# Kernel optimization log

Measured on AMD Instinct MI355X. Metric: run time of the kernel, lower is better.

The kernel has to match this reference:

```python
import jax, jax.numpy as jnp
import numpy as np

B, IN, H, E, N_EP, V_DIM = 4096, 1024, 16, 256, 2048, 64


def setup_inputs() -> dict:
    key = jax.random.key(0)
    k_x, k_c, k_w, k_k, k_v = jax.random.split(key, 5)
    x = jax.random.normal(k_x, (B, IN), dtype=jnp.float32)
    curiosity_score = jax.random.normal(k_c, (B,), dtype=jnp.float32)
    # toqueries: Linear(IN, E*H, bias=False); store as [IN, E*H] for x @ Wq
    Wq = jax.random.normal(k_w, (IN, E * H), dtype=jnp.float32) * (1.0 / np.sqrt(IN))
    # offline_keys [n_episodes, emb_size]; buffer repeats over heads (identical), so keep 2D
    keys = jax.random.normal(k_k, (N_EP, E), dtype=jnp.float32)
    # values buffer = offline_values.abs().mean(dim=-1) -> [n_episodes]
    offline_values = jax.random.normal(k_v, (N_EP, V_DIM), dtype=jnp.float32)
    values = jnp.abs(offline_values).mean(axis=-1)
    return {"x": x, "curiosity_score": curiosity_score, "Wq": Wq, "keys": keys, "values": values}


def reference(x, curiosity_score, Wq, keys, values):
    b = x.shape[0]
    # queries: [b, h, e], scaled by e**(1/4) (keys left unscaled, as in source)
    q = (x @ Wq).reshape(b, H, E) / (E ** 0.25)
    # dot: [b, h, n_episodes]; keys identical across heads -> single contraction
    dot = jnp.einsum("bhe,ne->bhn", q, keys) + values[None, None, :]
    dot = jax.nn.softmax(dot, axis=-1)
    # curiosity reweighting: scale probabilities then re-softmax (not scale-invariant)
    cur = jnp.exp(curiosity_score).reshape(b, 1, 1)
    dot = jax.nn.softmax(dot * cur, axis=-1)
    # head-mean -> [b, n_episodes]
    return dot.mean(axis=1)
```

## Files before the change

### kernel.cpp

```cpp
#include <hip/hip_runtime.h>


typedef __attribute__((ext_vector_type(8))) short bf16x8;
typedef __attribute__((ext_vector_type(4))) float f32x4;

typedef const __attribute__((address_space(1))) void* gcptr;
typedef __attribute__((address_space(3))) void* sptr;

__device__ __forceinline__ void gload16(const void* g, void* l) {
  __builtin_amdgcn_global_load_lds((gcptr)g, (sptr)l, 16, 0, 0);
}

__device__ __forceinline__ unsigned short f2bf(float f) {
  unsigned int u = __float_as_uint(f);
  unsigned int r = (u + 0x7fffu + ((u >> 16) & 1u)) >> 16;
  return (unsigned short)r;
}
__device__ __forceinline__ float bf2f(unsigned short s) {
  return __uint_as_float(((unsigned int)s) << 16);
}

__global__ void k_split(const float* __restrict__ src,
                        unsigned short* __restrict__ hi,
                        unsigned short* __restrict__ lo, int n4) {
  int i = blockIdx.x * blockDim.x + threadIdx.x;
  if (i >= n4) return;
  float4 v = reinterpret_cast<const float4*>(src)[i];
  ushort4 h, l;
  h.x = f2bf(v.x); l.x = f2bf(v.x - bf2f(h.x));
  h.y = f2bf(v.y); l.y = f2bf(v.y - bf2f(h.y));
  h.z = f2bf(v.z); l.z = f2bf(v.z - bf2f(h.z));
  h.w = f2bf(v.w); l.w = f2bf(v.w - bf2f(h.w));
  reinterpret_cast<ushort4*>(hi)[i] = h;
  reinterpret_cast<ushort4*>(lo)[i] = l;
}

__global__ void k_prepk(const float* __restrict__ keys,
                        unsigned short* __restrict__ th,
                        unsigned short* __restrict__ tl) {
  int g = blockIdx.x * blockDim.x + threadIdx.x;
  int k0 = g >> 13, rem = g & 8191;
  int jg = rem >> 6, lam = rem & 63;
  int row = jg * 16 + (lam & 15);
  int col = k0 * 32 + (lam >> 4) * 8;
  const float* s = keys + (size_t)row * 256 + col;
  float4 v0 = *reinterpret_cast<const float4*>(s);
  float4 v1 = *reinterpret_cast<const float4*>(s + 4);
  ushort4 h0, h1, l0, l1;
  h0.x = f2bf(v0.x); l0.x = f2bf(v0.x - bf2f(h0.x));
  h0.y = f2bf(v0.y); l0.y = f2bf(v0.y - bf2f(h0.y));
  h0.z = f2bf(v0.z); l0.z = f2bf(v0.z - bf2f(h0.z));
  h0.w = f2bf(v0.w); l0.w = f2bf(v0.w - bf2f(h0.w));
  h1.x = f2bf(v1.x); l1.x = f2bf(v1.x - bf2f(h1.x));
  h1.y = f2bf(v1.y); l1.y = f2bf(v1.y - bf2f(h1.y));
  h1.z = f2bf(v1.z); l1.z = f2bf(v1.z - bf2f(h1.z));
  h1.w = f2bf(v1.w); l1.w = f2bf(v1.w - bf2f(h1.w));
  reinterpret_cast<ushort4*>(th + (size_t)g * 8)[0] = h0;
  reinterpret_cast<ushort4*>(th + (size_t)g * 8)[1] = h1;
  reinterpret_cast<ushort4*>(tl + (size_t)g * 8)[0] = l0;
  reinterpret_cast<ushort4*>(tl + (size_t)g * 8)[1] = l1;
}

__global__ void k_twq(const float* __restrict__ W,
                      unsigned short* __restrict__ th,
                      unsigned short* __restrict__ tl) {
  __shared__ float t[64][65];
  int tx = threadIdx.x & 63, ty = threadIdx.x >> 6;
  int c0 = blockIdx.x * 64, r0 = blockIdx.y * 64;
#pragma unroll
  for (int i = 0; i < 64; i += 4)
    t[ty + i][tx] = W[(size_t)(r0 + ty + i) * 4096 + (c0 + tx)] * 0.25f;
  __syncthreads();
#pragma unroll
  for (int i = 0; i < 64; i += 4) {
    float v = t[tx][ty + i];
    unsigned short h = f2bf(v);
    unsigned short l = f2bf(v - bf2f(h));
    size_t o = (size_t)(c0 + ty + i) * 1024 + (r0 + tx);
    th[o] = h; tl[o] = l;
  }
}

__global__ __launch_bounds__(256) void k_gemm1(
    const unsigned short* __restrict__ Ah, const unsigned short* __restrict__ Al,
    const unsigned short* __restrict__ Bh, const unsigned short* __restrict__ Bl,
    unsigned short* __restrict__ Qh, unsigned short* __restrict__ Ql) {
  __shared__ unsigned short As[2][128][32];
  __shared__ unsigned short Bs[2][128][32];
  const int tid = threadIdx.x;
  const int w = tid >> 6, l = tid & 63;
  const int lr = l & 15, lg = l >> 4;
  const int m0 = blockIdx.y * 128, n0 = blockIdx.x * 128;
  const int wr = (w >> 1) * 64, wc = (w & 1) * 64;
  const int srow = tid >> 2;
  const int skel = (tid & 3) * 8;
  f32x4 acc[4][4] = {};

  const size_t gaBase = (size_t)(m0 + srow) * 1024 + skel;
  const size_t gbBase = (size_t)(n0 + srow) * 1024 + skel;
  char* lA0 = (char*)&As[0][0][0] + w * 1024;
  char* lA1 = (char*)&As[1][0][0] + w * 1024;
  char* lB0 = (char*)&Bs[0][0][0] + w * 1024;
  char* lB1 = (char*)&Bs[1][0][0] + w * 1024;

  for (int k0 = 0; k0 < 1024; k0 += 32) {
    gload16(Ah + gaBase + k0,             lA0);
    gload16(Ah + gaBase + 64 * 1024 + k0, lA0 + 4096);
    gload16(Al + gaBase + k0,             lA1);
    gload16(Al + gaBase + 64 * 1024 + k0, lA1 + 4096);
    gload16(Bh + gbBase + k0,             lB0);
    gload16(Bh + gbBase + 64 * 1024 + k0, lB0 + 4096);
    gload16(Bl + gbBase + k0,             lB1);
    gload16(Bl + gbBase + 64 * 1024 + k0, lB1 + 4096);
    __syncthreads();
    bf16x8 ah[4], am[4], bh[4], bm[4];
#pragma unroll
    for (int i = 0; i < 4; ++i) {
      ah[i] = *reinterpret_cast<const bf16x8*>(&As[0][wr + i * 16 + lr][lg * 8]);
      am[i] = *reinterpret_cast<const bf16x8*>(&As[1][wr + i * 16 + lr][lg * 8]);
      bh[i] = *reinterpret_cast<const bf16x8*>(&Bs[0][wc + i * 16 + lr][lg * 8]);
      bm[i] = *reinterpret_cast<const bf16x8*>(&Bs[1][wc + i * 16 + lr][lg * 8]);
    }
#pragma unroll
    for (int i = 0; i < 4; ++i)
#pragma unroll
      for (int j = 0; j < 4; ++j) {
        acc[i][j] = __builtin_amdgcn_mfma_f32_16x16x32_bf16(ah[i], bh[j], acc[i][j], 0, 0, 0);
        acc[i][j] = __builtin_amdgcn_mfma_f32_16x16x32_bf16(am[i], bh[j], acc[i][j], 0, 0, 0);
        acc[i][j] = __builtin_amdgcn_mfma_f32_16x16x32_bf16(ah[i], bm[j], acc[i][j], 0, 0, 0);
      }
    __syncthreads();
  }
#pragma unroll
  for (int i = 0; i < 4; ++i)
#pragma unroll
    for (int j = 0; j < 4; ++j)
#pragma unroll
      for (int r = 0; r < 4; ++r) {
        int row = m0 + wr + i * 16 + lg * 4 + r;
        int col = n0 + wc + j * 16 + lr;
        float v = acc[i][j][r];
        unsigned short hh = f2bf(v);
        unsigned short ll = f2bf(v - bf2f(hh));
        size_t o = (size_t)row * 4096 + col;
        Qh[o] = hh; Ql[o] = ll;
      }
}

#define MFMA_BF16(a, b, c) __builtin_amdgcn_mfma_f32_16x16x32_bf16(a, b, c, 0, 0, 0)

#define C_OF(T) ((unsigned)((((T) >> 4) * 128 + ((T) & 15)) * 1024))

#define LOADB(SLOT, T)                                                        \
  B##SLOT = *reinterpret_cast<const bf16x8*>(kHb + (vbase + C_OF(T)));        \
  L##SLOT = *reinterpret_cast<const bf16x8*>(kLb + (vbase + C_OF(T)));

#define JST(J, SLOT, PF, T)                          \
  __builtin_amdgcn_s_setprio(1);                     \
  acc[0][J] = MFMA_BF16(ah0, B##SLOT, acc[0][J]);    \
  acc[1][J] = MFMA_BF16(ah1, B##SLOT, acc[1][J]);    \
  acc[0][J] = MFMA_BF16(am0, B##SLOT, acc[0][J]);    \
  acc[1][J] = MFMA_BF16(am1, B##SLOT, acc[1][J]);    \
  acc[0][J] = MFMA_BF16(ah0, L##SLOT, acc[0][J]);    \
  acc[1][J] = MFMA_BF16(ah1, L##SLOT, acc[1][J]);    \
  __builtin_amdgcn_s_setprio(0);                     \
  if (PF) { LOADB(SLOT, T) }

#define BODY_HEAD(K)                                                   \
  ah0 = *reinterpret_cast<const bf16x8*>(As + ((K)) * 512 + l8);       \
  ah1 = *reinterpret_cast<const bf16x8*>(As + (8 + (K)) * 512 + l8);   \
  am0 = *reinterpret_cast<const bf16x8*>(As + (16 + (K)) * 512 + l8);  \
  am1 = *reinterpret_cast<const bf16x8*>(As + (24 + (K)) * 512 + l8);

#define BODY(K)                        \
  BODY_HEAD(K)                         \
  JST(0,  0, 1, (K) * 16 + 4)          \
  JST(1,  1, 1, (K) * 16 + 5)          \
  JST(2,  2, 1, (K) * 16 + 6)          \
  JST(3,  3, 1, (K) * 16 + 7)          \
  JST(4,  0, 1, (K) * 16 + 8)          \
  JST(5,  1, 1, (K) * 16 + 9)          \
  JST(6,  2, 1, (K) * 16 + 10)         \
  JST(7,  3, 1, (K) * 16 + 11)         \
  JST(8,  0, 1, (K) * 16 + 12)         \
  JST(9,  1, 1, (K) * 16 + 13)         \
  JST(10, 2, 1, (K) * 16 + 14)         \
  JST(11, 3, 1, (K) * 16 + 15)         \
  JST(12, 0, 1, (K) * 16 + 16)         \
  JST(13, 1, 1, (K) * 16 + 17)         \
  JST(14, 2, 1, (K) * 16 + 18)         \
  JST(15, 3, 1, (K) * 16 + 19)

#define BODY7            \
  BODY_HEAD(7)           \
  JST(0,  0, 1, 116)     \
  JST(1,  1, 1, 117)     \
  JST(2,  2, 1, 118)     \
  JST(3,  3, 1, 119)     \
  JST(4,  0, 1, 120)     \
  JST(5,  1, 1, 121)     \
  JST(6,  2, 1, 122)     \
  JST(7,  3, 1, 123)     \
  JST(8,  0, 1, 124)     \
  JST(9,  1, 1, 125)     \
  JST(10, 2, 1, 126)     \
  JST(11, 3, 1, 127)     \
  JST(12, 0, 0, 0)       \
  JST(13, 1, 0, 0)       \
  JST(14, 2, 0, 0)       \
  JST(15, 3, 0, 0)

__global__ __launch_bounds__(512, 2) void k_attn(
    const unsigned short* __restrict__ Qh, const unsigned short* __restrict__ Ql,
    const unsigned short* __restrict__ KtH, const unsigned short* __restrict__ KtL,
    const float* __restrict__ values, const float* __restrict__ cur,
    float* __restrict__ out) {
  __shared__ unsigned short As[32 * 512];
  __shared__ float red[8][32];
  const int tid = threadIdx.x;
  const int w = tid >> 6, l = tid & 63;
  const int lr = l & 15, lg = l >> 4;
  const int r0 = blockIdx.x * 32;
  const int cs = (int)((w + blockIdx.x) & 7);
  const int n0 = cs * 256;
  const int l8 = l * 8;

#pragma unroll
  for (int qq = 0; qq < 4; ++qq) {
    const int s = w * 4 + qq;
    const int plane = s >> 4, mf = (s >> 3) & 1, k0s = s & 7;
    const unsigned short* src = plane ? Ql : Qh;
    const size_t ga = (size_t)(r0 + mf * 16 + lr) * 256 + k0s * 32 + lg * 8;
    gload16(src + ga, (char*)As + s * 1024);
  }
  __syncthreads();

  const unsigned sliceB = (unsigned)__builtin_amdgcn_readfirstlane(cs * 16384);
  const char* kHb = (const char*)KtH + sliceB;
  const char* kLb = (const char*)KtL + sliceB;
  const unsigned vbase = (unsigned)(l * 16);

  f32x4 acc[2][16] = {};
  bf16x8 B0, B1, B2, B3, L0, L1, L2, L3;
  bf16x8 ah0, ah1, am0, am1;

  LOADB(0, 0) LOADB(1, 1) LOADB(2, 2) LOADB(3, 3)

  BODY(0) BODY(1) BODY(2) BODY(3) BODY(4) BODY(5) BODY(6) BODY7

#pragma unroll
  for (int j = 0; j < 16; ++j) {
    float vv = values[n0 + j * 16 + lr];
#pragma unroll
    for (int mf = 0; mf < 2; ++mf)
#pragma unroll
      for (int r = 0; r < 4; ++r) acc[mf][j][r] += vv;
  }

  const int rb = lg * 4;
  float M1[2][4];
#pragma unroll
  for (int mf = 0; mf < 2; ++mf)
#pragma unroll
    for (int r = 0; r < 4; ++r) {
      float m = acc[mf][0][r];
#pragma unroll
      for (int j = 1; j < 16; ++j) m = fmaxf(m, acc[mf][j][r]);
      m = fmaxf(m, __shfl_xor(m, 1));
      m = fmaxf(m, __shfl_xor(m, 2));
      m = fmaxf(m, __shfl_xor(m, 4));
      m = fmaxf(m, __shfl_xor(m, 8));
      M1[mf][r] = m;
    }
  if (lr == 0) {
#pragma unroll
    for (int mf = 0; mf < 2; ++mf)
#pragma unroll
      for (int r = 0; r < 4; ++r) red[w][mf * 16 + rb + r] = M1[mf][r];
  }
  __syncthreads();
#pragma unroll
  for (int mf = 0; mf < 2; ++mf)
#pragma unroll
    for (int r = 0; r < 4; ++r) {
      float m = red[0][mf * 16 + rb + r];
#pragma unroll
      for (int w2 = 1; w2 < 8; ++w2) m = fmaxf(m, red[w2][mf * 16 + rb + r]);
      M1[mf][r] = m;
    }
  __syncthreads();
  float Z1[2][4];
#pragma unroll
  for (int mf = 0; mf < 2; ++mf)
#pragma unroll
    for (int r = 0; r < 4; ++r) {
      float z = 0.f;
#pragma unroll
      for (int j = 0; j < 16; ++j) {
        float e = __expf(acc[mf][j][r] - M1[mf][r]);
        acc[mf][j][r] = e;
        z += e;
      }
      z += __shfl_xor(z, 1); z += __shfl_xor(z, 2);
      z += __shfl_xor(z, 4); z += __shfl_xor(z, 8);
      Z1[mf][r] = z;
    }
  if (lr == 0) {
#pragma unroll
    for (int mf = 0; mf < 2; ++mf)
#pragma unroll
      for (int r = 0; r < 4; ++r) red[w][mf * 16 + rb + r] = Z1[mf][r];
  }
  __syncthreads();
#pragma unroll
  for (int mf = 0; mf < 2; ++mf)
#pragma unroll
    for (int r = 0; r < 4; ++r) {
      float z = 0.f;
#pragma unroll
      for (int w2 = 0; w2 < 8; ++w2) z += red[w2][mf * 16 + rb + r];
      Z1[mf][r] = z;
    }
  __syncthreads();
  const float c0 = __expf(cur[(r0 >> 4) + 0]);
  const float c1 = __expf(cur[(r0 >> 4) + 1]);
  float Z2[2][4];
#pragma unroll
  for (int mf = 0; mf < 2; ++mf)
#pragma unroll
    for (int r = 0; r < 4; ++r) {
      float s2 = (mf ? c1 : c0) / Z1[mf][r];
      float z = 0.f;
#pragma unroll
      for (int j = 0; j < 16; ++j) {
        float o = __expf(s2 * (acc[mf][j][r] - 1.0f));
        acc[mf][j][r] = o;
        z += o;
      }
      z += __shfl_xor(z, 1); z += __shfl_xor(z, 2);
      z += __shfl_xor(z, 4); z += __shfl_xor(z, 8);
      Z2[mf][r] = z;
    }
  if (lr == 0) {
#pragma unroll
    for (int mf = 0; mf < 2; ++mf)
#pragma unroll
      for (int r = 0; r < 4; ++r) red[w][mf * 16 + rb + r] = Z2[mf][r];
  }
  __syncthreads();
#pragma unroll
  for (int mf = 0; mf < 2; ++mf)
#pragma unroll
    for (int r = 0; r < 4; ++r) {
      float z = 0.f;
#pragma unroll
      for (int w2 = 0; w2 < 8; ++w2) z += red[w2][mf * 16 + rb + r];
      Z2[mf][r] = z;
    }
  float rz[2][4];
#pragma unroll
  for (int mf = 0; mf < 2; ++mf)
#pragma unroll
    for (int r = 0; r < 4; ++r) rz[mf][r] = 1.0f / (16.0f * Z2[mf][r]);
#pragma unroll
  for (int mf = 0; mf < 2; ++mf)
#pragma unroll
    for (int j = 0; j < 16; ++j) {
      float s = acc[mf][j][0] * rz[mf][0] + acc[mf][j][1] * rz[mf][1] +
                acc[mf][j][2] * rz[mf][2] + acc[mf][j][3] * rz[mf][3];
      s += __shfl_xor(s, 16);
      s += __shfl_xor(s, 32);
      if (l < 16)
        out[(size_t)((r0 >> 4) + mf) * 2048 + n0 + j * 16 + l] = s;
    }
}

extern "C" void kernel_launch(void* const* d_in, const int* in_sizes, int n_in,
                              void* d_out, int out_size, void* d_ws, size_t ws_size,
                              hipStream_t stream) {
  const float* x    = (const float*)d_in[0];
  const float* cur  = (const float*)d_in[1];
  const float* Wq   = (const float*)d_in[2];
  const float* keys = (const float*)d_in[3];
  const float* vals = (const float*)d_in[4];
  float* out = (float*)d_out;

  char* ws = (char*)d_ws;
  unsigned short* x_hi = (unsigned short*)ws;  ws += (size_t)4096 * 1024 * 2;
  unsigned short* x_lo = (unsigned short*)ws;  ws += (size_t)4096 * 1024 * 2;
  unsigned short* w_hi = (unsigned short*)ws;  ws += (size_t)4096 * 1024 * 2;
  unsigned short* w_lo = (unsigned short*)ws;  ws += (size_t)4096 * 1024 * 2;
  unsigned short* k_hi = (unsigned short*)ws;  ws += (size_t)2048 * 256 * 2;
  unsigned short* k_lo = (unsigned short*)ws;  ws += (size_t)2048 * 256 * 2;
  unsigned short* q_hi = (unsigned short*)ws;  ws += (size_t)4096 * 4096 * 2;
  unsigned short* q_lo = (unsigned short*)ws;

  k_split<<<4096, 256, 0, stream>>>(x, x_hi, x_lo, 4096 * 1024 / 4);
  k_prepk<<<256, 256, 0, stream>>>(keys, k_hi, k_lo);
  k_twq<<<dim3(64, 16), 256, 0, stream>>>(Wq, w_hi, w_lo);
  k_gemm1<<<dim3(32, 32), 256, 0, stream>>>(x_hi, x_lo, w_hi, w_lo, q_hi, q_lo);
  k_attn<<<2048, 512, 0, stream>>>(q_hi, q_lo, k_hi, k_lo, vals, cur, out);
}
```

Before: 377.2 us.

## Interleave key hi/lo planes into one buffer and drop MFMA priority hints

The key preparation kernel now writes the bf16 hi and lo parts of each key fragment next to each other in a single buffer (lo sits 1024 bytes after hi) instead of two separate arrays. The attention kernel then reads both B operands from one base pointer with a fixed offset, which saves address registers and keeps each pair of loads close together in memory. The s_setprio raise and lower around each MFMA group are also removed, which changes wave scheduling and may alter how loads and MFMAs overlap.

```diff
diff --git a/kernel.cpp b/kernel.cpp
--- a/kernel.cpp
+++ b/kernel.cpp
@@ -36,8 +36,7 @@
 }
 
 __global__ void k_prepk(const float* __restrict__ keys,
-                        unsigned short* __restrict__ th,
-                        unsigned short* __restrict__ tl) {
+                        unsigned short* __restrict__ kt) {
   int g = blockIdx.x * blockDim.x + threadIdx.x;
   int k0 = g >> 13, rem = g & 8191;
   int jg = rem >> 6, lam = rem & 63;
@@ -55,10 +54,11 @@
   h1.y = f2bf(v1.y); l1.y = f2bf(v1.y - bf2f(h1.y));
   h1.z = f2bf(v1.z); l1.z = f2bf(v1.z - bf2f(h1.z));
   h1.w = f2bf(v1.w); l1.w = f2bf(v1.w - bf2f(h1.w));
-  reinterpret_cast<ushort4*>(th + (size_t)g * 8)[0] = h0;
-  reinterpret_cast<ushort4*>(th + (size_t)g * 8)[1] = h1;
-  reinterpret_cast<ushort4*>(tl + (size_t)g * 8)[0] = l0;
-  reinterpret_cast<ushort4*>(tl + (size_t)g * 8)[1] = l1;
+  size_t base = (size_t)(k0 * 128 + jg) * 1024 + lam * 8;
+  reinterpret_cast<ushort4*>(kt + base)[0] = h0;
+  reinterpret_cast<ushort4*>(kt + base)[1] = h1;
+  reinterpret_cast<ushort4*>(kt + base + 512)[0] = l0;
+  reinterpret_cast<ushort4*>(kt + base + 512)[1] = l1;
 }
 
 __global__ void k_twq(const float* __restrict__ W,
@@ -149,21 +149,22 @@
 
 #define MFMA_BF16(a, b, c) __builtin_amdgcn_mfma_f32_16x16x32_bf16(a, b, c, 0, 0, 0)
 
-#define C_OF(T) ((unsigned)((((T) >> 4) * 128 + ((T) & 15)) * 1024))
-
-#define LOADB(SLOT, T)                                                        \
-  B##SLOT = *reinterpret_cast<const bf16x8*>(kHb + (vbase + C_OF(T)));        \
-  L##SLOT = *reinterpret_cast<const bf16x8*>(kLb + (vbase + C_OF(T)));
+#define C_OF(T) ((unsigned)((((T) >> 4) * 262144) + (((T) & 15) * 2048)))
+
+#define LOADB(SLOT, T)                                                   \
+  {                                                                      \
+    const char* p = kb + (vbase + C_OF(T));                              \
+    B##SLOT = *reinterpret_cast<const bf16x8*>(p);                       \
+    L##SLOT = *reinterpret_cast<const bf16x8*>(p + 1024);                \
+  }
 
 #define JST(J, SLOT, PF, T)                          \
-  __builtin_amdgcn_s_setprio(1);                     \
   acc[0][J] = MFMA_BF16(ah0, B##SLOT, acc[0][J]);    \
   acc[1][J] = MFMA_BF16(ah1, B##SLOT, acc[1][J]);    \
   acc[0][J] = MFMA_BF16(am0, B##SLOT, acc[0][J]);    \
   acc[1][J] = MFMA_BF16(am1, B##SLOT, acc[1][J]);    \
   acc[0][J] = MFMA_BF16(ah0, L##SLOT, acc[0][J]);    \
   acc[1][J] = MFMA_BF16(ah1, L##SLOT, acc[1][J]);    \
-  __builtin_amdgcn_s_setprio(0);                     \
   if (PF) { LOADB(SLOT, T) }
 
 #define BODY_HEAD(K)                                                   \
@@ -212,7 +213,7 @@
 
 __global__ __launch_bounds__(512, 2) void k_attn(
     const unsigned short* __restrict__ Qh, const unsigned short* __restrict__ Ql,
-    const unsigned short* __restrict__ KtH, const unsigned short* __restrict__ KtL,
+    const unsigned short* __restrict__ Kt,
     const float* __restrict__ values, const float* __restrict__ cur,
     float* __restrict__ out) {
   __shared__ unsigned short As[32 * 512];
@@ -235,9 +236,8 @@
   }
   __syncthreads();
 
-  const unsigned sliceB = (unsigned)__builtin_amdgcn_readfirstlane(cs * 16384);
-  const char* kHb = (const char*)KtH + sliceB;
-  const char* kLb = (const char*)KtL + sliceB;
+  const unsigned sliceB = (unsigned)__builtin_amdgcn_readfirstlane(cs * 32768);
+  const char* kb = (const char*)Kt + sliceB;
   const unsigned vbase = (unsigned)(l * 16);
 
   f32x4 acc[2][16] = {};
@@ -390,14 +390,13 @@
   unsigned short* x_lo = (unsigned short*)ws;  ws += (size_t)4096 * 1024 * 2;
   unsigned short* w_hi = (unsigned short*)ws;  ws += (size_t)4096 * 1024 * 2;
   unsigned short* w_lo = (unsigned short*)ws;  ws += (size_t)4096 * 1024 * 2;
-  unsigned short* k_hi = (unsigned short*)ws;  ws += (size_t)2048 * 256 * 2;
-  unsigned short* k_lo = (unsigned short*)ws;  ws += (size_t)2048 * 256 * 2;
+  unsigned short* k_t  = (unsigned short*)ws;  ws += (size_t)2048 * 256 * 2 * 2;
   unsigned short* q_hi = (unsigned short*)ws;  ws += (size_t)4096 * 4096 * 2;
   unsigned short* q_lo = (unsigned short*)ws;
 
   k_split<<<4096, 256, 0, stream>>>(x, x_hi, x_lo, 4096 * 1024 / 4);
-  k_prepk<<<256, 256, 0, stream>>>(keys, k_hi, k_lo);
+  k_prepk<<<256, 256, 0, stream>>>(keys, k_t);
   k_twq<<<dim3(64, 16), 256, 0, stream>>>(Wq, w_hi, w_lo);
   k_gemm1<<<dim3(32, 32), 256, 0, stream>>>(x_hi, x_lo, w_hi, w_lo, q_hi, q_lo);
-  k_attn<<<2048, 512, 0, stream>>>(q_hi, q_lo, k_hi, k_lo, vals, cur, out);
-}
+  k_attn<<<2048, 512, 0, stream>>>(q_hi, q_lo, k_t, vals, cur, out);
+}
```

After: 481.2 us. 27.6% more time.
